# Optimization experiments

Measured on AMD Instinct MI355X. Metric: run time of the kernel, lower is better.

## Reference

```python
import jax, jax.numpy as jnp
import numpy as np

N = 50000   # n_nodes (cells)
E = 800000  # n_edges (avg degree 16)
D = 128     # feature dim


def setup_inputs() -> dict:
    key = jax.random.key(0)
    ks = jax.random.split(key, 8)
    x = jax.random.normal(ks[0], (N, D), dtype=jnp.float32)
    src = jax.random.randint(ks[1], (E,), 0, N, dtype=jnp.int32)
    dst = jax.random.randint(ks[2], (E,), 0, N, dtype=jnp.int32)
    vals = jax.random.uniform(ks[3], (E,), dtype=jnp.float32)
    # GraphConvolution weight (dim -> dim), applied as x @ W
    W_gc = jax.random.normal(ks[4], (D, D), dtype=jnp.float32) / np.sqrt(D).astype(np.float32)
    b_gc = jnp.zeros((D,), jnp.float32)
    # linear2: nn.Linear(dim, dim) -> x @ W2.T + b2
    W2 = jax.random.normal(ks[5], (D, D), dtype=jnp.float32) / np.sqrt(D).astype(np.float32)
    b2 = jnp.zeros((D,), jnp.float32)
    return {"x": x, "vals": vals, "W_gc": W_gc, "b_gc": b_gc,
            "W2": W2, "b2": b2, "src": src, "dst": dst}


def reference(x, vals, W_gc, b_gc, W2, b2, src, dst):
    # GraphConvolution (dropout is identity in eval mode):
    #   support = x @ W + b ; out = relu(adj_sparse @ support)
    support = x @ W_gc + b_gc                         # [N, D]
    msg = support[src] * vals[:, None]                # gather rows, scale by edge weight
    agg = jax.ops.segment_sum(msg, dst, num_segments=N)  # SpMM via scatter-add
    x1 = jax.nn.relu(agg)                             # [N, D]
    # linear2 + dropout(eval=identity) + detached L2 row-normalize
    x2 = x1 @ W2.T + b2                               # [N, D]
    nrm = jax.lax.stop_gradient(
        jnp.sqrt(jnp.sum(x2 * x2, axis=1, keepdims=True)))
    return x2 / nrm
```

## Files before the change

### kernel.cpp

```cpp
#include <hip/hip_runtime.h>
#include <hip/hip_bf16.h>

#define N_NODES 50000
#define N_EDGES 800000
#define DIM     128
#define N_STRIPS (N_NODES / 16)
#define N_BKT    ((N_NODES + 255) / 256)
#define EDGE_BLOCKS ((N_EDGES + 4095) / 4096)
#define BUF_CAP  6144
#define GEMM_BLOCKS ((N_STRIPS + 3) / 4)
#define HIST_BLOCK0 GEMM_BLOCKS
#define PACK_BLOCK0 (GEMM_BLOCKS + EDGE_BLOCKS)
#define FRONT_BLOCKS (PACK_BLOCK0 + 16)

typedef short short8 __attribute__((ext_vector_type(8)));
typedef float floatx4 __attribute__((ext_vector_type(4)));

__device__ inline unsigned short f2bf(float f) {
    __hip_bfloat16 h = __float2bfloat16(f);
    return *reinterpret_cast<unsigned short*>(&h);
}

__global__ __launch_bounds__(256) void fused_front(
    const float* __restrict__ x, const float* __restrict__ W,
    const float* __restrict__ W2, const float* __restrict__ bias,
    const int* __restrict__ dst,
    unsigned short* __restrict__ support, int* __restrict__ blk_hist,
    uint4* __restrict__ p1, uint4* __restrict__ p2)
{
    __shared__ int bh[256];
    const int t = threadIdx.x;

    if (blockIdx.x < HIST_BLOCK0) {
        const int wave  = t >> 6;
        const int lane  = t & 63;
        const int strip = blockIdx.x * 4 + wave;
        if (strip >= N_STRIPS) return;
        const int m = lane & 15;
        const int q = lane >> 4;
        const int row = strip * 16 + m;

        short8 a[4];
        const float4* xr = reinterpret_cast<const float4*>(&x[(size_t)row * DIM]);
        #pragma unroll
        for (int ks = 0; ks < 4; ++ks) {
            const float4 f0 = xr[ks * 8 + q * 2];
            const float4 f1 = xr[ks * 8 + q * 2 + 1];
            short8 tt;
            tt[0] = (short)f2bf(f0.x); tt[1] = (short)f2bf(f0.y);
            tt[2] = (short)f2bf(f0.z); tt[3] = (short)f2bf(f0.w);
            tt[4] = (short)f2bf(f1.x); tt[5] = (short)f2bf(f1.y);
            tt[6] = (short)f2bf(f1.z); tt[7] = (short)f2bf(f1.w);
            a[ks] = tt;
        }

        floatx4 acc[8];
        #pragma unroll
        for (int nt = 0; nt < 8; ++nt) { acc[nt][0]=0.f; acc[nt][1]=0.f; acc[nt][2]=0.f; acc[nt][3]=0.f; }

        const short8* Bp = (const short8*)p1;
        #pragma unroll
        for (int ks = 0; ks < 4; ++ks) {
            #pragma unroll
            for (int nt = 0; nt < 8; ++nt) {
                const short8 bf = Bp[(ks * 8 + nt) * 64 + lane];
                acc[nt] = __builtin_amdgcn_mfma_f32_16x16x32_bf16(a[ks], bf, acc[nt], 0, 0, 0);
            }
        }

        #pragma unroll
        for (int nt = 0; nt < 8; ++nt) {
            const float bb = bias[nt * 16 + m];
            #pragma unroll
            for (int i = 0; i < 4; ++i) {
                const int r = strip * 16 + q * 4 + i;
                support[(size_t)r * DIM + nt * 16 + m] = f2bf(acc[nt][i] + bb);
            }
        }
    } else if (blockIdx.x < PACK_BLOCK0) {
        const int chunk = blockIdx.x - HIST_BLOCK0;
        bh[t] = 0;
        __syncthreads();
        const int base   = chunk * 4096;
        const int navail = min(4096, N_EDGES - base);
        const int4* d4 = reinterpret_cast<const int4*>(dst + base);
        #pragma unroll
        for (int i = 0; i < 4; ++i) {
            const int j = t + i * 256;
            if (j * 4 < navail) {
                const int4 d = d4[j];
                atomicAdd(&bh[d.x >> 8], 1);
                atomicAdd(&bh[d.y >> 8], 1);
                atomicAdd(&bh[d.z >> 8], 1);
                atomicAdd(&bh[d.w >> 8], 1);
            }
        }
        __syncthreads();
        blk_hist[chunk * 256 + t] = bh[t];
    } else {
        const int pb   = blockIdx.x - PACK_BLOCK0;
        const int s    = (pb & 7) * 256 + t;
        const int lane = s & 63;
        const int nt   = (s >> 6) & 7;
        const int ks   = s >> 9;
        const int m    = lane & 15;
        const int q    = lane >> 4;

        unsigned short e[8];
        if (pb < 8) {
            #pragma unroll
            for (int j = 0; j < 8; ++j)
                e[j] = f2bf(W[(ks * 32 + q * 8 + j) * DIM + nt * 16 + m]);
            uint4 o;
            o.x = (unsigned)e[0] | ((unsigned)e[1] << 16);
            o.y = (unsigned)e[2] | ((unsigned)e[3] << 16);
            o.z = (unsigned)e[4] | ((unsigned)e[5] << 16);
            o.w = (unsigned)e[6] | ((unsigned)e[7] << 16);
            p1[s] = o;
        } else {
            const float4 f0 = *reinterpret_cast<const float4*>(&W2[(nt * 16 + m) * DIM + ks * 32 + q * 8]);
            const float4 f1 = *reinterpret_cast<const float4*>(&W2[(nt * 16 + m) * DIM + ks * 32 + q * 8 + 4]);
            e[0] = f2bf(f0.x); e[1] = f2bf(f0.y); e[2] = f2bf(f0.z); e[3] = f2bf(f0.w);
            e[4] = f2bf(f1.x); e[5] = f2bf(f1.y); e[6] = f2bf(f1.z); e[7] = f2bf(f1.w);
            uint4 o;
            o.x = (unsigned)e[0] | ((unsigned)e[1] << 16);
            o.y = (unsigned)e[2] | ((unsigned)e[3] << 16);
            o.z = (unsigned)e[4] | ((unsigned)e[5] << 16);
            o.w = (unsigned)e[6] | ((unsigned)e[7] << 16);
            p2[s] = o;
        }
    }
}


__global__ __launch_bounds__(256) void pack_w1(
    const float* __restrict__ W, uint4* __restrict__ p1)
{
    const int s    = blockIdx.x * 256 + threadIdx.x;
    const int lane = s & 63;
    const int nt   = (s >> 6) & 7;
    const int ks   = s >> 9;
    const int m    = lane & 15;
    const int q    = lane >> 4;
    unsigned short e[8];
    #pragma unroll
    for (int j = 0; j < 8; ++j)
        e[j] = f2bf(W[(ks * 32 + q * 8 + j) * DIM + nt * 16 + m]);
    uint4 o;
    o.x = (unsigned)e[0] | ((unsigned)e[1] << 16);
    o.y = (unsigned)e[2] | ((unsigned)e[3] << 16);
    o.z = (unsigned)e[4] | ((unsigned)e[5] << 16);
    o.w = (unsigned)e[6] | ((unsigned)e[7] << 16);
    p1[s] = o;
}

__global__ __launch_bounds__(1024) void scan_hist(
    const int* __restrict__ blk_hist, int* __restrict__ blk_base,
    int* __restrict__ bbase)
{
    __shared__ int psum[4][256];
    __shared__ int stot[256];
    __shared__ int sinc[256];

    const int t    = threadIdx.x;
    const int b    = t & 255;
    const int part = t >> 8;
    const int c0   = part * 49;
    const int c1   = min(c0 + 49, EDGE_BLOCKS);

    int run = 0;
    #pragma unroll 7
    for (int c = c0; c < c1; ++c) {
        const int v = blk_hist[c * 256 + b];
        blk_base[c * 256 + b] = run;
        run += v;
    }
    psum[part][b] = run;
    __syncthreads();

    if (part == 0) {
        const int tot = psum[0][b] + psum[1][b] + psum[2][b] + psum[3][b];
        stot[b] = tot;
        sinc[b] = tot;
    }
    __syncthreads();
    for (int off = 1; off < 256; off <<= 1) {
        int u = 0;
        if (part == 0 && b >= off) u = sinc[b - off];
        __syncthreads();
        if (part == 0 && b >= off) sinc[b] += u;
        __syncthreads();
    }
    const int ex = sinc[b] - stot[b];
    if (part == 0 && b < N_BKT) bbase[b] = ex;
    if (t == 0) bbase[N_BKT] = N_EDGES;

    int partbase = 0;
    #pragma unroll
    for (int p = 0; p < 4; ++p) if (p < part) partbase += psum[p][b];
    const int add = ex + partbase;
    #pragma unroll 7
    for (int c = c0; c < c1; ++c) blk_base[c * 256 + b] += add;
}

__global__ __launch_bounds__(256) void bucket_scatter(
    const int* __restrict__ src, const int* __restrict__ dst,
    const float* __restrict__ vals, const int* __restrict__ blk_base,
    int2* __restrict__ bucketed)
{
    __shared__ int rcur[256];
    const int t     = threadIdx.x;
    const int chunk = blockIdx.x;
    rcur[t] = blk_base[chunk * 256 + t];
    __syncthreads();

    const int base   = chunk * 4096;
    const int navail = min(4096, N_EDGES - base);
    const int4*   s4 = reinterpret_cast<const int4*>(src + base);
    const int4*   d4 = reinterpret_cast<const int4*>(dst + base);
    const float4* v4 = reinterpret_cast<const float4*>(vals + base);
    #pragma unroll
    for (int i = 0; i < 4; ++i) {
        const int j = t + i * 256;
        if (j * 4 < navail) {
            const int4   s = s4[j];
            const int4   d = d4[j];
            const float4 v = v4[j];
            int p;
            p = atomicAdd(&rcur[d.x >> 8], 1);
            bucketed[p] = make_int2((s.x & 0xFFFF) | ((d.x & 0xFF) << 16), __float_as_int(v.x));
            p = atomicAdd(&rcur[d.y >> 8], 1);
            bucketed[p] = make_int2((s.y & 0xFFFF) | ((d.y & 0xFF) << 16), __float_as_int(v.y));
            p = atomicAdd(&rcur[d.z >> 8], 1);
            bucketed[p] = make_int2((s.z & 0xFFFF) | ((d.z & 0xFF) << 16), __float_as_int(v.z));
            p = atomicAdd(&rcur[d.w >> 8], 1);
            bucketed[p] = make_int2((s.w & 0xFFFF) | ((d.w & 0xFF) << 16), __float_as_int(v.w));
        }
    }
}

__global__ __launch_bounds__(256) void bucket_to_csr(
    const int2* __restrict__ bucketed, const int* __restrict__ bbase,
    int2* __restrict__ packed, int* __restrict__ offs)
{
    __shared__ int cnt[256];
    __shared__ int sc[256];
    __shared__ int lcur[256];
    __shared__ int2 buf[BUF_CAP];

    const int b    = blockIdx.x;
    const int t    = threadIdx.x;
    const int base = bbase[b];
    const int nE   = bbase[b + 1] - base;

    cnt[t] = 0;
    __syncthreads();
    for (int i = t; i < nE; i += 256)
        atomicAdd(&cnt[(bucketed[base + i].x >> 16) & 0xFF], 1);
    __syncthreads();
    sc[t] = cnt[t];
    __syncthreads();
    #pragma unroll
    for (int off = 1; off < 256; off <<= 1) {
        int u = (t >= off) ? sc[t - off] : 0;
        __syncthreads();
        sc[t] += u;
        __syncthreads();
    }
    const int ex = sc[t] - cnt[t];
    lcur[t] = ex;
    __syncthreads();

    if (nE <= BUF_CAP) {
        for (int i = t; i < nE; i += 256) {
            const int2 e = bucketed[base + i];
            const int  n = (e.x >> 16) & 0xFF;
            const int  p = atomicAdd(&lcur[n], 1);
            buf[p] = make_int2(e.x & 0xFFFF, e.y);
        }
        __syncthreads();
        for (int i = t; i < nE; i += 256)
            packed[base + i] = buf[i];
    } else {
        for (int i = t; i < nE; i += 256) {
            const int2 e = bucketed[base + i];
            const int  n = (e.x >> 16) & 0xFF;
            const int  p = atomicAdd(&lcur[n], 1);
            packed[base + p] = make_int2(e.x & 0xFFFF, e.y);
        }
    }

    const int node = b * 256 + t;
    if (node < N_NODES) offs[node] = base + ex;
    if (b == N_BKT - 1 && t == 0) offs[N_NODES] = N_EDGES;
}

__global__ __launch_bounds__(256) void csr_gather_bf16(
    const unsigned int* __restrict__ sup, const int2* __restrict__ packed,
    const int* __restrict__ offs, unsigned int* __restrict__ agg)
{
    const int node = (blockIdx.x * 256 + threadIdx.x) >> 6;
    const int lane = threadIdx.x & 63;
    if (node >= N_NODES) return;
    const int beg = offs[node];
    const int end = offs[node + 1];

    float ax = 0.f, ay = 0.f;
    int j = beg;
    for (; j + 3 < end; j += 4) {
        const int2 e0 = packed[j];
        const int2 e1 = packed[j + 1];
        const int2 e2 = packed[j + 2];
        const int2 e3 = packed[j + 3];
        const unsigned int u0 = sup[(size_t)e0.x * 64 + lane];
        const unsigned int u1 = sup[(size_t)e1.x * 64 + lane];
        const unsigned int u2 = sup[(size_t)e2.x * 64 + lane];
        const unsigned int u3 = sup[(size_t)e3.x * 64 + lane];
        const float v0 = __int_as_float(e0.y);
        const float v1 = __int_as_float(e1.y);
        const float v2 = __int_as_float(e2.y);
        const float v3 = __int_as_float(e3.y);
        ax += __uint_as_float(u0 << 16) * v0;          ay += __uint_as_float(u0 & 0xffff0000u) * v0;
        ax += __uint_as_float(u1 << 16) * v1;          ay += __uint_as_float(u1 & 0xffff0000u) * v1;
        ax += __uint_as_float(u2 << 16) * v2;          ay += __uint_as_float(u2 & 0xffff0000u) * v2;
        ax += __uint_as_float(u3 << 16) * v3;          ay += __uint_as_float(u3 & 0xffff0000u) * v3;
    }
    for (; j < end; ++j) {
        const int2 e0 = packed[j];
        const unsigned int u0 = sup[(size_t)e0.x * 64 + lane];
        const float v0 = __int_as_float(e0.y);
        ax += __uint_as_float(u0 << 16) * v0;
        ay += __uint_as_float(u0 & 0xffff0000u) * v0;
    }
    ax = fmaxf(ax, 0.f);
    ay = fmaxf(ay, 0.f);
    agg[(size_t)node * 64 + lane] = (unsigned int)f2bf(ax) | ((unsigned int)f2bf(ay) << 16);
}

__global__ __launch_bounds__(256) void gemm2_mfma(
    const short8* __restrict__ aggv, const short8* __restrict__ Bp,
    const float* __restrict__ bias, float* __restrict__ out)
{
    const int wave  = threadIdx.x >> 6;
    const int lane  = threadIdx.x & 63;
    const int strip = blockIdx.x * 4 + wave;
    if (strip >= N_STRIPS) return;
    const int m = lane & 15;
    const int q = lane >> 4;
    const int row = strip * 16 + m;

    short8 a[4];
    #pragma unroll
    for (int ks = 0; ks < 4; ++ks)
        a[ks] = aggv[(size_t)row * (DIM / 8) + ks * 4 + q];

    floatx4 acc[8];
    #pragma unroll
    for (int nt = 0; nt < 8; ++nt) { acc[nt][0]=0.f; acc[nt][1]=0.f; acc[nt][2]=0.f; acc[nt][3]=0.f; }

    #pragma unroll
    for (int ks = 0; ks < 4; ++ks) {
        #pragma unroll
        for (int nt = 0; nt < 8; ++nt) {
            const short8 bf = Bp[(ks * 8 + nt) * 64 + lane];
            acc[nt] = __builtin_amdgcn_mfma_f32_16x16x32_bf16(a[ks], bf, acc[nt], 0, 0, 0);
        }
    }

    #pragma unroll
    for (int nt = 0; nt < 8; ++nt) {
        const float bb = bias[nt * 16 + m];
        #pragma unroll
        for (int i = 0; i < 4; ++i) acc[nt][i] += bb;
    }

    float sq[4] = {0.f, 0.f, 0.f, 0.f};
    #pragma unroll
    for (int nt = 0; nt < 8; ++nt)
        #pragma unroll
        for (int i = 0; i < 4; ++i) sq[i] += acc[nt][i] * acc[nt][i];
    #pragma unroll
    for (int i = 0; i < 4; ++i) {
        #pragma unroll
        for (int mask = 1; mask < 16; mask <<= 1)
            sq[i] += __shfl_xor(sq[i], mask);
        sq[i] = 1.0f / sqrtf(sq[i]);
    }

    #pragma unroll
    for (int nt = 0; nt < 8; ++nt) {
        #pragma unroll
        for (int i = 0; i < 4; ++i) {
            const int r = strip * 16 + q * 4 + i;
            out[(size_t)r * DIM + nt * 16 + m] = acc[nt][i] * sq[i];
        }
    }
}

extern "C" void kernel_launch(void* const* d_in, const int* in_sizes, int n_in,
                              void* d_out, int out_size, void* d_ws, size_t ws_size,
                              hipStream_t stream) {
    const float* x    = (const float*)d_in[0];
    const float* vals = (const float*)d_in[1];
    const float* W_gc = (const float*)d_in[2];
    const float* b_gc = (const float*)d_in[3];
    const float* W2   = (const float*)d_in[4];
    const float* b2   = (const float*)d_in[5];
    const int*   src  = (const int*)d_in[6];
    const int*   dst  = (const int*)d_in[7];

    unsigned short* support = (unsigned short*)d_out;
    float* out = (float*)d_out;

    const size_t AGG_B  = (size_t)N_NODES * DIM * 2;
    const size_t OFFS_B = 200064;
    const size_t BH_B   = (size_t)EDGE_BLOCKS * 256 * 4;
    const size_t BB_B   = (size_t)EDGE_BLOCKS * 256 * 4;
    const size_t BKT_B  = 1024;
    const size_t BUK_B  = (size_t)N_EDGES * 8;
    const size_t PACK_B = (size_t)N_EDGES * 8;
    const size_t PW_B   = 32768;

    char* wsb = (char*)d_ws;
    unsigned int* agg = (unsigned int*)wsb;
    int*   offs     = (int*)(wsb + AGG_B);
    int*   blk_hist = (int*)(wsb + AGG_B + OFFS_B);
    int*   blk_base = (int*)(wsb + AGG_B + OFFS_B + BH_B);
    int*   bbase    = (int*)(wsb + AGG_B + OFFS_B + BH_B + BB_B);
    int2*  bucketed = (int2*)(wsb + AGG_B + OFFS_B + BH_B + BB_B + BKT_B);
    int2*  packed   = (int2*)(wsb + AGG_B + OFFS_B + BH_B + BB_B + BKT_B + BUK_B);
    uint4* pw1      = (uint4*)(wsb + AGG_B + OFFS_B + BH_B + BB_B + BKT_B + BUK_B + PACK_B);
    uint4* pw2      = (uint4*)(wsb + AGG_B + OFFS_B + BH_B + BB_B + BKT_B + BUK_B + PACK_B + PW_B);

    pack_w1<<<8, 256, 0, stream>>>(W_gc, pw1);

    fused_front<<<FRONT_BLOCKS, 256, 0, stream>>>(
        x, W_gc, W2, b_gc, dst, support, blk_hist, pw1, pw2);

    scan_hist<<<1, 1024, 0, stream>>>(blk_hist, blk_base, bbase);

    bucket_scatter<<<EDGE_BLOCKS, 256, 0, stream>>>(src, dst, vals, blk_base, bucketed);

    bucket_to_csr<<<N_BKT, 256, 0, stream>>>(bucketed, bbase, packed, offs);

    csr_gather_bf16<<<(N_NODES * 64 + 255) / 256, 256, 0, stream>>>(
        (const unsigned int*)support, packed, offs, agg);

    gemm2_mfma<<<(N_STRIPS + 3) / 4, 256, 0, stream>>>(
        (const short8*)agg, (const short8*)pw2, b2, out);
}
```

Baseline: 181.0 us.

## Fuse CSR gather with second GEMM via LDS slab, widen bucket_to_csr blocks

The CSR gather and the second MFMA GEMM are merged into one kernel. Each wave aggregates 16 rows into an LDS slab and then runs the GEMM on that slab directly, so the bf16 aggregate no longer makes a round trip through global memory. The support buffer moves from the output buffer into the workspace, since the output is now written by the fused kernel. bucket_to_csr goes to 512 threads, scan_hist keeps its prefixes in registers instead of re-reading blk_base, and the W1 pack is removed from fused_front. The trade-off is less parallelism in the gather, because one wave now handles 16 nodes in sequence instead of one node per wave, and the whole block waits at a barrier.

```diff
diff --git a/kernel.cpp b/kernel.cpp
--- a/kernel.cpp
+++ b/kernel.cpp
@@ -12,6 +12,7 @@
 #define HIST_BLOCK0 GEMM_BLOCKS
 #define PACK_BLOCK0 (GEMM_BLOCKS + EDGE_BLOCKS)
 #define FRONT_BLOCKS (PACK_BLOCK0 + 16)
+#define CHUNKS_PER_PART (EDGE_BLOCKS / 4)
 
 typedef short short8 __attribute__((ext_vector_type(8)));
 typedef float floatx4 __attribute__((ext_vector_type(4)));
@@ -21,12 +22,33 @@
     return *reinterpret_cast<unsigned short*>(&h);
 }
 
+__global__ __launch_bounds__(256) void pack_w1(
+    const float* __restrict__ W, uint4* __restrict__ p1)
+{
+    const int s    = blockIdx.x * 256 + threadIdx.x;
+    const int lane = s & 63;
+    const int nt   = (s >> 6) & 7;
+    const int ks   = s >> 9;
+    const int m    = lane & 15;
+    const int q    = lane >> 4;
+    unsigned short e[8];
+    #pragma unroll
+    for (int j = 0; j < 8; ++j)
+        e[j] = f2bf(W[(ks * 32 + q * 8 + j) * DIM + nt * 16 + m]);
+    uint4 o;
+    o.x = (unsigned)e[0] | ((unsigned)e[1] << 16);
+    o.y = (unsigned)e[2] | ((unsigned)e[3] << 16);
+    o.z = (unsigned)e[4] | ((unsigned)e[5] << 16);
+    o.w = (unsigned)e[6] | ((unsigned)e[7] << 16);
+    p1[s] = o;
+}
+
 __global__ __launch_bounds__(256) void fused_front(
-    const float* __restrict__ x, const float* __restrict__ W,
-    const float* __restrict__ W2, const float* __restrict__ bias,
-    const int* __restrict__ dst,
+    const float* __restrict__ x, const float* __restrict__ W2,
+    const float* __restrict__ bias, const int* __restrict__ dst,
+    const uint4* __restrict__ p1,
     unsigned short* __restrict__ support, int* __restrict__ blk_hist,
-    uint4* __restrict__ p1, uint4* __restrict__ p2)
+    uint4* __restrict__ p2)
 {
     __shared__ int bh[256];
     const int t = threadIdx.x;
@@ -100,58 +122,24 @@
     } else {
         const int pb   = blockIdx.x - PACK_BLOCK0;
         const int s    = (pb & 7) * 256 + t;
+        if (pb >= 8) return;
         const int lane = s & 63;
         const int nt   = (s >> 6) & 7;
         const int ks   = s >> 9;
         const int m    = lane & 15;
         const int q    = lane >> 4;
-
+        const float4 f0 = *reinterpret_cast<const float4*>(&W2[(nt * 16 + m) * DIM + ks * 32 + q * 8]);
+        const float4 f1 = *reinterpret_cast<const float4*>(&W2[(nt * 16 + m) * DIM + ks * 32 + q * 8 + 4]);
         unsigned short e[8];
-        if (pb < 8) {
-            #pragma unroll
-            for (int j = 0; j < 8; ++j)
-                e[j] = f2bf(W[(ks * 32 + q * 8 + j) * DIM + nt * 16 + m]);
-            uint4 o;
-            o.x = (unsigned)e[0] | ((unsigned)e[1] << 16);
-            o.y = (unsigned)e[2] | ((unsigned)e[3] << 16);
-            o.z = (unsigned)e[4] | ((unsigned)e[5] << 16);
-            o.w = (unsigned)e[6] | ((unsigned)e[7] << 16);
-            p1[s] = o;
-        } else {
-            const float4 f0 = *reinterpret_cast<const float4*>(&W2[(nt * 16 + m) * DIM + ks * 32 + q * 8]);
-            const float4 f1 = *reinterpret_cast<const float4*>(&W2[(nt * 16 + m) * DIM + ks * 32 + q * 8 + 4]);
-            e[0] = f2bf(f0.x); e[1] = f2bf(f0.y); e[2] = f2bf(f0.z); e[3] = f2bf(f0.w);
-            e[4] = f2bf(f1.x); e[5] = f2bf(f1.y); e[6] = f2bf(f1.z); e[7] = f2bf(f1.w);
-            uint4 o;
-            o.x = (unsigned)e[0] | ((unsigned)e[1] << 16);
-            o.y = (unsigned)e[2] | ((unsigned)e[3] << 16);
-            o.z = (unsigned)e[4] | ((unsigned)e[5] << 16);
-            o.w = (unsigned)e[6] | ((unsigned)e[7] << 16);
-            p2[s] = o;
-        }
-    }
-}
-
-
-__global__ __launch_bounds__(256) void pack_w1(
-    const float* __restrict__ W, uint4* __restrict__ p1)
-{
-    const int s    = blockIdx.x * 256 + threadIdx.x;
-    const int lane = s & 63;
-    const int nt   = (s >> 6) & 7;
-    const int ks   = s >> 9;
-    const int m    = lane & 15;
-    const int q    = lane >> 4;
-    unsigned short e[8];
-    #pragma unroll
-    for (int j = 0; j < 8; ++j)
-        e[j] = f2bf(W[(ks * 32 + q * 8 + j) * DIM + nt * 16 + m]);
-    uint4 o;
-    o.x = (unsigned)e[0] | ((unsigned)e[1] << 16);
-    o.y = (unsigned)e[2] | ((unsigned)e[3] << 16);
-    o.z = (unsigned)e[4] | ((unsigned)e[5] << 16);
-    o.w = (unsigned)e[6] | ((unsigned)e[7] << 16);
-    p1[s] = o;
+        e[0] = f2bf(f0.x); e[1] = f2bf(f0.y); e[2] = f2bf(f0.z); e[3] = f2bf(f0.w);
+        e[4] = f2bf(f1.x); e[5] = f2bf(f1.y); e[6] = f2bf(f1.z); e[7] = f2bf(f1.w);
+        uint4 o;
+        o.x = (unsigned)e[0] | ((unsigned)e[1] << 16);
+        o.y = (unsigned)e[2] | ((unsigned)e[3] << 16);
+        o.z = (unsigned)e[4] | ((unsigned)e[5] << 16);
+        o.w = (unsigned)e[6] | ((unsigned)e[7] << 16);
+        p2[s] = o;
+    }
 }
 
 __global__ __launch_bounds__(1024) void scan_hist(
@@ -165,14 +153,14 @@
     const int t    = threadIdx.x;
     const int b    = t & 255;
     const int part = t >> 8;
-    const int c0   = part * 49;
-    const int c1   = min(c0 + 49, EDGE_BLOCKS);
-
+    const int c0   = part * CHUNKS_PER_PART;
+
+    int pre[CHUNKS_PER_PART];
     int run = 0;
-    #pragma unroll 7
-    for (int c = c0; c < c1; ++c) {
-        const int v = blk_hist[c * 256 + b];
-        blk_base[c * 256 + b] = run;
+    #pragma unroll
+    for (int k = 0; k < CHUNKS_PER_PART; ++k) {
+        const int v = blk_hist[(c0 + k) * 256 + b];
+        pre[k] = run;
         run += v;
     }
     psum[part][b] = run;
@@ -199,8 +187,9 @@
     #pragma unroll
     for (int p = 0; p < 4; ++p) if (p < part) partbase += psum[p][b];
     const int add = ex + partbase;
-    #pragma unroll 7
-    for (int c = c0; c < c1; ++c) blk_base[c * 256 + b] += add;
+    #pragma unroll
+    for (int k = 0; k < CHUNKS_PER_PART; ++k)
+        blk_base[(c0 + k) * 256 + b] = pre[k] + add;
 }
 
 __global__ __launch_bounds__(256) void bucket_scatter(
@@ -239,7 +228,7 @@
     }
 }
 
-__global__ __launch_bounds__(256) void bucket_to_csr(
+__global__ __launch_bounds__(512) void bucket_to_csr(
     const int2* __restrict__ bucketed, const int* __restrict__ bbase,
     int2* __restrict__ packed, int* __restrict__ offs)
 {
@@ -253,36 +242,36 @@
     const int base = bbase[b];
     const int nE   = bbase[b + 1] - base;
 
-    cnt[t] = 0;
-    __syncthreads();
-    for (int i = t; i < nE; i += 256)
+    if (t < 256) cnt[t] = 0;
+    __syncthreads();
+    for (int i = t; i < nE; i += 512)
         atomicAdd(&cnt[(bucketed[base + i].x >> 16) & 0xFF], 1);
     __syncthreads();
-    sc[t] = cnt[t];
+    if (t < 256) sc[t] = cnt[t];
     __syncthreads();
     #pragma unroll
     for (int off = 1; off < 256; off <<= 1) {
-        int u = (t >= off) ? sc[t - off] : 0;
-        __syncthreads();
-        sc[t] += u;
-        __syncthreads();
-    }
-    const int ex = sc[t] - cnt[t];
-    lcur[t] = ex;
+        int u = 0;
+        if (t < 256 && t >= off) u = sc[t - off];
+        __syncthreads();
+        if (t < 256 && t >= off) sc[t] += u;
+        __syncthreads();
+    }
+    if (t < 256) lcur[t] = sc[t] - cnt[t];
     __syncthreads();
 
     if (nE <= BUF_CAP) {
-        for (int i = t; i < nE; i += 256) {
+        for (int i = t; i < nE; i += 512) {
             const int2 e = bucketed[base + i];
             const int  n = (e.x >> 16) & 0xFF;
             const int  p = atomicAdd(&lcur[n], 1);
             buf[p] = make_int2(e.x & 0xFFFF, e.y);
         }
         __syncthreads();
-        for (int i = t; i < nE; i += 256)
+        for (int i = t; i < nE; i += 512)
             packed[base + i] = buf[i];
     } else {
-        for (int i = t; i < nE; i += 256) {
+        for (int i = t; i < nE; i += 512) {
             const int2 e = bucketed[base + i];
             const int  n = (e.x >> 16) & 0xFF;
             const int  p = atomicAdd(&lcur[n], 1);
@@ -290,69 +279,70 @@
         }
     }
 
-    const int node = b * 256 + t;
-    if (node < N_NODES) offs[node] = base + ex;
+    if (t < 256) {
+        const int node = b * 256 + t;
+        if (node < N_NODES) offs[node] = base + (sc[t] - cnt[t]);
+    }
     if (b == N_BKT - 1 && t == 0) offs[N_NODES] = N_EDGES;
 }
 
-__global__ __launch_bounds__(256) void csr_gather_bf16(
+__global__ __launch_bounds__(256) void gather_gemm2(
     const unsigned int* __restrict__ sup, const int2* __restrict__ packed,
-    const int* __restrict__ offs, unsigned int* __restrict__ agg)
-{
-    const int node = (blockIdx.x * 256 + threadIdx.x) >> 6;
+    const int* __restrict__ offs, const short8* __restrict__ Bp,
+    const float* __restrict__ bias, float* __restrict__ out)
+{
+    __shared__ __align__(16) unsigned short slab[4][16][136];
+
+    const int wave = threadIdx.x >> 6;
     const int lane = threadIdx.x & 63;
-    if (node >= N_NODES) return;
-    const int beg = offs[node];
-    const int end = offs[node + 1];
-
-    float ax = 0.f, ay = 0.f;
-    int j = beg;
-    for (; j + 3 < end; j += 4) {
-        const int2 e0 = packed[j];
-        const int2 e1 = packed[j + 1];
-        const int2 e2 = packed[j + 2];
-        const int2 e3 = packed[j + 3];
-        const unsigned int u0 = sup[(size_t)e0.x * 64 + lane];
-        const unsigned int u1 = sup[(size_t)e1.x * 64 + lane];
-        const unsigned int u2 = sup[(size_t)e2.x * 64 + lane];
-        const unsigned int u3 = sup[(size_t)e3.x * 64 + lane];
-        const float v0 = __int_as_float(e0.y);
-        const float v1 = __int_as_float(e1.y);
-        const float v2 = __int_as_float(e2.y);
-        const float v3 = __int_as_float(e3.y);
-        ax += __uint_as_float(u0 << 16) * v0;          ay += __uint_as_float(u0 & 0xffff0000u) * v0;
-        ax += __uint_as_float(u1 << 16) * v1;          ay += __uint_as_float(u1 & 0xffff0000u) * v1;
-        ax += __uint_as_float(u2 << 16) * v2;          ay += __uint_as_float(u2 & 0xffff0000u) * v2;
-        ax += __uint_as_float(u3 << 16) * v3;          ay += __uint_as_float(u3 & 0xffff0000u) * v3;
-    }
-    for (; j < end; ++j) {
-        const int2 e0 = packed[j];
-        const unsigned int u0 = sup[(size_t)e0.x * 64 + lane];
-        const float v0 = __int_as_float(e0.y);
-        ax += __uint_as_float(u0 << 16) * v0;
-        ay += __uint_as_float(u0 & 0xffff0000u) * v0;
-    }
-    ax = fmaxf(ax, 0.f);
-    ay = fmaxf(ay, 0.f);
-    agg[(size_t)node * 64 + lane] = (unsigned int)f2bf(ax) | ((unsigned int)f2bf(ay) << 16);
-}
-
-__global__ __launch_bounds__(256) void gemm2_mfma(
-    const short8* __restrict__ aggv, const short8* __restrict__ Bp,
-    const float* __restrict__ bias, float* __restrict__ out)
-{
-    const int wave  = threadIdx.x >> 6;
-    const int lane  = threadIdx.x & 63;
-    const int strip = blockIdx.x * 4 + wave;
-    if (strip >= N_STRIPS) return;
+    int strip = blockIdx.x * 4 + wave;
+    if (strip >= N_STRIPS) strip = N_STRIPS - 1;
+
+    for (int i = 0; i < 16; ++i) {
+        const int node = strip * 16 + i;
+        const int beg = offs[node];
+        const int end = offs[node + 1];
+        float ax = 0.f, ay = 0.f;
+        int j = beg;
+        for (; j + 3 < end; j += 4) {
+            const int2 e0 = packed[j];
+            const int2 e1 = packed[j + 1];
+            const int2 e2 = packed[j + 2];
+            const int2 e3 = packed[j + 3];
+            const unsigned int u0 = sup[(size_t)e0.x * 64 + lane];
+            const unsigned int u1 = sup[(size_t)e1.x * 64 + lane];
+            const unsigned int u2 = sup[(size_t)e2.x * 64 + lane];
+            const unsigned int u3 = sup[(size_t)e3.x * 64 + lane];
+            const float v0 = __int_as_float(e0.y);
+            const float v1 = __int_as_float(e1.y);
+            const float v2 = __int_as_float(e2.y);
+            const float v3 = __int_as_float(e3.y);
+            ax += __uint_as_float(u0 << 16) * v0;  ay += __uint_as_float(u0 & 0xffff0000u) * v0;
+            ax += __uint_as_float(u1 << 16) * v1;  ay += __uint_as_float(u1 & 0xffff0000u) * v1;
+            ax += __uint_as_float(u2 << 16) * v2;  ay += __uint_as_float(u2 & 0xffff0000u) * v2;
+            ax += __uint_as_float(u3 << 16) * v3;  ay += __uint_as_float(u3 & 0xffff0000u) * v3;
+        }
+        for (; j < end; ++j) {
+            const int2 e0 = packed[j];
+            const unsigned int u0 = sup[(size_t)e0.x * 64 + lane];
+            const float v0 = __int_as_float(e0.y);
+            ax += __uint_as_float(u0 << 16) * v0;
+            ay += __uint_as_float(u0 & 0xffff0000u) * v0;
+        }
+        ax = fmaxf(ax, 0.f);
+        ay = fmaxf(ay, 0.f);
+        *reinterpret_cast<unsigned int*>(&slab[wave][i][2 * lane]) =
+            (unsigned int)f2bf(ax) | ((unsigned int)f2bf(ay) << 16);
+    }
+    __syncthreads();
+
     const int m = lane & 15;
     const int q = lane >> 4;
-    const int row = strip * 16 + m;
 
     short8 a[4];
     #pragma unroll
     for (int ks = 0; ks < 4; ++ks)
-        a[ks] = aggv[(size_t)row * (DIM / 8) + ks * 4 + q];
+        a[ks] = *reinterpret_cast<const short8*>(&slab[wave][m][ks * 32 + q * 8]);
 
     floatx4 acc[8];
     #pragma unroll
@@ -409,10 +399,9 @@
     const int*   src  = (const int*)d_in[6];
     const int*   dst  = (const int*)d_in[7];
 
-    unsigned short* support = (unsigned short*)d_out;
     float* out = (float*)d_out;
 
-    const size_t AGG_B  = (size_t)N_NODES * DIM * 2;
+    const size_t SUP_B  = (size_t)N_NODES * DIM * 2;
     const size_t OFFS_B = 200064;
     const size_t BH_B   = (size_t)EDGE_BLOCKS * 256 * 4;
     const size_t BB_B   = (size_t)EDGE_BLOCKS * 256 * 4;
@@ -422,30 +411,28 @@
     const size_t PW_B   = 32768;
 
     char* wsb = (char*)d_ws;
-    unsigned int* agg = (unsigned int*)wsb;
-    int*   offs     = (int*)(wsb + AGG_B);
-    int*   blk_hist = (int*)(wsb + AGG_B + OFFS_B);
-    int*   blk_base = (int*)(wsb + AGG_B + OFFS_B + BH_B);
-    int*   bbase    = (int*)(wsb + AGG_B + OFFS_B + BH_B + BB_B);
-    int2*  bucketed = (int2*)(wsb + AGG_B + OFFS_B + BH_B + BB_B + BKT_B);
-    int2*  packed   = (int2*)(wsb + AGG_B + OFFS_B + BH_B + BB_B + BKT_B + BUK_B);
-    uint4* pw1      = (uint4*)(wsb + AGG_B + OFFS_B + BH_B + BB_B + BKT_B + BUK_B + PACK_B);
-    uint4* pw2      = (uint4*)(wsb + AGG_B + OFFS_B + BH_B + BB_B + BKT_B + BUK_B + PACK_B + PW_B);
+    unsigned short* support = (unsigned short*)wsb;
+    int*   offs     = (int*)(wsb + SUP_B);
+    int*   blk_hist = (int*)(wsb + SUP_B + OFFS_B);
+    int*   blk_base = (int*)(wsb + SUP_B + OFFS_B + BH_B);
+    int*   bbase    = (int*)(wsb + SUP_B + OFFS_B + BH_B + BB_B);
+    int2*  bucketed = (int2*)(wsb + SUP_B + OFFS_B + BH_B + BB_B + BKT_B);
+    int2*  packed   = (int2*)(wsb + SUP_B + OFFS_B + BH_B + BB_B + BKT_B + BUK_B);
+    uint4* pw1      = (uint4*)(wsb + SUP_B + OFFS_B + BH_B + BB_B + BKT_B + BUK_B + PACK_B);
+    uint4* pw2      = (uint4*)(wsb + SUP_B + OFFS_B + BH_B + BB_B + BKT_B + BUK_B + PACK_B + PW_B);
 
     pack_w1<<<8, 256, 0, stream>>>(W_gc, pw1);
 
     fused_front<<<FRONT_BLOCKS, 256, 0, stream>>>(
-        x, W_gc, W2, b_gc, dst, support, blk_hist, pw1, pw2);
+        x, W2, b_gc, dst, pw1, support, blk_hist, pw2);
 
     scan_hist<<<1, 1024, 0, stream>>>(blk_hist, blk_base, bbase);
 
     bucket_scatter<<<EDGE_BLOCKS, 256, 0, stream>>>(src, dst, vals, blk_base, bucketed);
 
-    bucket_to_csr<<<N_BKT, 256, 0, stream>>>(bucketed, bbase, packed, offs);
-
-    csr_gather_bf16<<<(N_NODES * 64 + 255) / 256, 256, 0, stream>>>(
-        (const unsigned int*)support, packed, offs, agg);
-
-    gemm2_mfma<<<(N_STRIPS + 3) / 4, 256, 0, stream>>>(
-        (const short8*)agg, (const short8*)pw2, b2, out);
-}
+    bucket_to_csr<<<N_BKT, 512, 0, stream>>>(bucketed, bbase, packed, offs);
+
+    gather_gemm2<<<GEMM_BLOCKS, 256, 0, stream>>>(
+        (const unsigned int*)support, packed, offs,
+        (const short8*)pw2, b2, out);
+}
```

Result: slower. 195.4 us (+7.9%).
